# Kernel tuning notes

Measured on AMD Instinct MI355X. Metric: run time of the kernel, lower is better.

The kernel has to match this reference:

```python
import jax, jax.numpy as jnp
import numpy as np

B, S, T, H, D = 4, 128, 128, 256, 3


def setup_inputs() -> dict:
    key = jax.random.key(0)
    ks = jax.random.split(key, 10)
    s = 1.0 / np.sqrt(H).astype(np.float32)
    return {
        "src": jax.random.normal(ks[0], (B, S, H), jnp.float32),
        "trg": jax.random.normal(ks[1], (B, T, H), jnp.float32),
        "Wx_ih": jax.random.normal(ks[2], (D, H, H), jnp.float32) * s,
        "Wx_hh": jax.random.normal(ks[3], (D, H, H), jnp.float32) * s,
        "bx_ih": jax.random.normal(ks[4], (D, H), jnp.float32) * s,
        "bx_hh": jax.random.normal(ks[5], (D, H), jnp.float32) * s,
        "Wy_ih": jax.random.normal(ks[6], (D, H, H), jnp.float32) * s,
        "Wy_hh": jax.random.normal(ks[7], (D, H, H), jnp.float32) * s,
        "by_ih": jax.random.normal(ks[8], (D, H), jnp.float32) * s,
        "by_hh": jax.random.normal(ks[9], (D, H), jnp.float32) * s,
    }


def _grid_rnn(src, trg, Wx_ih, Wx_hh, bx_ih, bx_hh, Wy_ih, Wy_hh, by_ih, by_hh):
    dt = src.dtype
    hx = hy = None
    for d in range(D):
        if d == 0:
            xin = jnp.broadcast_to(src[:, :, None, :], (B, S, T, H))  # x_t(i,j)=src[i]
            yin = jnp.broadcast_to(trg[:, None, :, :], (B, S, T, H))  # y_t(i,j)=trg[j]
        else:
            xin, yin = hx, hy  # outputs of previous depth

        # ---- h_x: recurrence over rows i; state_x(i,j) = h_x(i-1, j-1),
        # with j==0 reading index -2 (Python wraparound) = h_x(i-1, T-1) -> jnp.roll.
        Wih, Whh, bih, bhh = Wx_ih[d], Wx_hh[d], bx_ih[d], bx_hh[d]

        def step_x(carry, x_i, Wih=Wih, Whh=Whh, bih=bih, bhh=bhh):
            state = jnp.roll(carry, 1, axis=1)  # [B,T,H]: state[j] = carry[j-1]
            h = jnp.tanh(x_i @ Wih.T + bih + state @ Whh.T + bhh)
            return h, h

        _, hx = jax.lax.scan(step_x, jnp.zeros((B, T, H), dt), jnp.swapaxes(xin, 0, 1))
        hx = jnp.swapaxes(hx, 0, 1)  # [B,S,T,H]

        # ---- h_y: recurrence over columns j; state_y(i,j) = h_y(i, j-1); rows independent.
        Wihy, Whhy, bihy, bhhy = Wy_ih[d], Wy_hh[d], by_ih[d], by_hh[d]

        def step_y(carry, y_j, Wih=Wihy, Whh=Whhy, bih=bihy, bhh=bhhy):
            h = jnp.tanh(y_j @ Wih.T + bih + carry @ Whh.T + bhh)
            return h, h

        _, hy = jax.lax.scan(step_y, jnp.zeros((B, S, H), dt), jnp.moveaxis(yin, 2, 0))
        hy = jnp.moveaxis(hy, 0, 2)  # [B,S,T,H]

    # final-depth output grid: slot 2j = h_x, slot 2j+1 = h_y
    return jnp.stack([hx, hy], axis=-2)  # [B,S,T,2,H]


def reference(src, trg, Wx_ih, Wx_hh, bx_ih, bx_hh, Wy_ih, Wy_hh, by_ih, by_hh):
    return _grid_rnn(src, trg, Wx_ih, Wx_hh, bx_ih, bx_hh, Wy_ih, Wy_hh, by_ih, by_hh)
```

## Files before the change

### kernel.cpp

```cpp
#include <hip/hip_runtime.h>


#define SS 128
#define TT 128
#define HH 256
#define GRID_ELEMS ((size_t)4 * 128 * 128 * 256)

typedef _Float16 half8 __attribute__((ext_vector_type(8)));
typedef float float4v __attribute__((ext_vector_type(4)));
typedef float float2v __attribute__((ext_vector_type(2)));

__device__ __forceinline__ float fast_tanh(float x) {
    float e = __expf(2.0f * x);
    return 1.0f - 2.0f / (e + 1.0f);
}

__device__ __forceinline__ unsigned short f2hbits(float x) {
    _Float16 h = (_Float16)x;
    return __builtin_bit_cast(unsigned short, h);
}

__device__ __forceinline__ float sel4(float4v v, int q) {
    float a = (q & 1) ? v[1] : v[0];
    float b = (q & 1) ? v[3] : v[2];
    return (q & 2) ? b : a;
}

__device__ __forceinline__ void lds_barrier() {
    asm volatile("s_waitcnt lgkmcnt(0)" ::: "memory");
    __builtin_amdgcn_s_barrier();
}

__device__ __forceinline__ half8 ldfrag_f32(const float* rowp, int k) {
    const float4v u0 = *(const float4v*)(rowp + k);
    const float4v u1 = *(const float4v*)(rowp + k + 4);
    half8 v;
#pragma unroll
    for (int e = 0; e < 4; ++e) { v[e] = (_Float16)u0[e]; v[4 + e] = (_Float16)u1[e]; }
    return v;
}

extern "C" __global__ void __launch_bounds__(512, 2)
grid_gemm0(const float* __restrict__ src, const float* __restrict__ trg,
           const float* __restrict__ Wx_ih, const float* __restrict__ Wy_ih,
           const float* __restrict__ bx_ih, const float* __restrict__ bx_hh,
           const float* __restrict__ by_ih, const float* __restrict__ by_hh,
           float* __restrict__ P0)
{
    __shared__ half8 aT[2048];

    const int tid  = threadIdx.x;
    const int lane = tid & 63;
    const int wv   = tid >> 6;
    const int quad = lane >> 4;
    const int l15  = lane & 15;

    const int bx    = blockIdx.x;
    const int dir   = bx >> 3;
    const int mtile = bx & 7;

    const float* Wih = dir ? Wy_ih : Wx_ih;
    const float* bih = dir ? by_ih : bx_ih;
    const float* bhh = dir ? by_hh : bx_hh;

    const int n_0 = (wv << 5) + l15;
    const int n_1 = n_0 + 16;

    half8 B0[8], B1[8];
    {
        const float* r0 = Wih + (size_t)n_0 * HH;
        const float* r1 = Wih + (size_t)n_1 * HH;
#pragma unroll
        for (int f = 0; f < 8; ++f) {
            const int k = (f << 5) + (quad << 3);
            B0[f] = ldfrag_f32(r0, k);
            B1[f] = ldfrag_f32(r1, k);
        }
    }
    const float bias0 = bih[n_0] + bhh[n_0];
    const float bias1 = bih[n_1] + bhh[n_1];

#pragma unroll
    for (int i = 0; i < 4; ++i) {
        const int c  = (tid << 2) + i;
        const int r  = c >> 5;
        const int kc = c & 31;
        const int R  = (mtile << 6) + r;
        const int b  = R >> 7, ii = R & 127;
        const float* row = (dir ? trg : src) + (size_t)((b << 7) + ii) * HH + (kc << 3);
        const float4v u0 = *(const float4v*)(row);
        const float4v u1 = *(const float4v*)(row + 4);
        half8 v;
#pragma unroll
        for (int e = 0; e < 4; ++e) { v[e] = (_Float16)u0[e]; v[4 + e] = (_Float16)u1[e]; }
        aT[((r >> 4) << 9) + ((kc >> 2) << 6) + ((kc & 3) << 4) + (r & 15)] = v;
    }
    __syncthreads();

#pragma unroll
    for (int msub = 0; msub < 4; ++msub) {
        half8 af[8];
#pragma unroll
        for (int f = 0; f < 8; ++f)
            af[f] = aT[(msub << 9) + (f << 6) + (quad << 4) + l15];

        float4v c0 = {bias0, bias0, bias0, bias0};
        float4v c1 = {bias1, bias1, bias1, bias1};
#pragma unroll
        for (int f = 0; f < 8; ++f) {
            c0 = __builtin_amdgcn_mfma_f32_16x16x32_f16(af[f], B0[f], c0, 0, 0, 0);
            c1 = __builtin_amdgcn_mfma_f32_16x16x32_f16(af[f], B1[f], c1, 0, 0, 0);
        }
#pragma unroll
        for (int r = 0; r < 4; ++r) {
            const int row = (msub << 4) + (quad << 2) + r;
            float* p = P0 + (size_t)dir * 131072 + (size_t)((mtile << 6) + row) * HH;
            p[n_0] = c0[r];
            p[n_1] = c1[r];
        }
    }
}

template <int DI>
__device__ __forceinline__ void rnn2f_body(
    const float* __restrict__ Wx_hh, const float* __restrict__ Wy_hh,
    const float* __restrict__ Wx_ih, const float* __restrict__ Wy_ih,
    const float* __restrict__ bx_ih, const float* __restrict__ bx_hh,
    const float* __restrict__ by_ih, const float* __restrict__ by_hh,
    float* __restrict__ out, const float* __restrict__ P0)
{
    __shared__ half8 aH[2][128];

    const int tid  = threadIdx.x;
    const int lane = tid & 63;
    const int wv   = tid >> 6;
    const int quad = lane >> 4;
    const int l15  = lane & 15;
    const int lrow = lane & 3;

    const int bid  = blockIdx.x;
    const int isY  = bid >= 128;
    const int g    = isY ? bid - 128 : bid;
    const int b    = g >> 5;
    const int c0   = (g & 31) << 2;
    const int slot = isY;

    const float* Whh  = (isY ? Wy_hh : Wx_hh) + (size_t)DI * HH * HH;
    const float* WihN = (isY ? Wy_ih : Wx_ih) + (size_t)(DI + 1) * HH * HH;
    const float* bihN = (isY ? by_ih : bx_ih) + (DI + 1) * HH;
    const float* bhhN = (isY ? by_hh : bx_hh) + (DI + 1) * HH;

    const int n_0 = (wv << 5) + l15;
    const int n_1 = n_0 + 16;

    half8 Bhh0[8], Bhh1[8], BN0[8], BN1[8];
    {
        const float* h0p = Whh  + (size_t)n_0 * HH;
        const float* h1p = Whh  + (size_t)n_1 * HH;
        const float* i0p = WihN + (size_t)n_0 * HH;
        const float* i1p = WihN + (size_t)n_1 * HH;
#pragma unroll
        for (int f = 0; f < 8; ++f) {
            const int k = (f << 5) + (quad << 3);
            Bhh0[f] = ldfrag_f32(h0p, k);
            Bhh1[f] = ldfrag_f32(h1p, k);
            BN0[f]  = ldfrag_f32(i0p, k);
            BN1[f]  = ldfrag_f32(i1p, k);
        }
    }
    const float biasN0 = bihN[n_0] + bhhN[n_0];
    const float biasN1 = bihN[n_1] + bhhN[n_1];

    int wj = isY ? 0 : ((c0 + quad) & 127);
    float* wp = out + (isY ? ((size_t)(b * SS + c0 + quad) * TT)
                           : ((size_t)b * SS * TT + wj)) * 2 * HH
                    + (size_t)slot * HH;

    float pA[4], pB[4];
    int rj = isY ? 0 : ((c0 + quad) & 127);
    const float* rp;
    if constexpr (DI == 0) {
        rp = P0 + (size_t)isY * 131072 + (size_t)b * 128 * HH;
    } else {
        rp = out + (isY ? ((size_t)(b * SS + c0 + quad) * TT)
                        : ((size_t)b * SS * TT + rj)) * 2 * HH
                 + (size_t)slot * HH;
    }
    auto rbump = [&]() {
        if constexpr (DI == 0) { rp += HH; }
        else if (isY)          { rp += 2 * HH; }
        else { rp += (size_t)(rj == 127 ? 1 : 129) * 2 * HH; rj = (rj + 1) & 127; }
    };
#pragma unroll
    for (int u = 0; u < 4; ++u) { pA[u] = rp[n_0]; pB[u] = rp[n_1]; rbump(); }

    if (tid < 128) {
        half8 z;
#pragma unroll
        for (int e = 0; e < 8; ++e) z[e] = (_Float16)0.f;
        aH[0][tid] = z;
    }
    __syncthreads();

    const int hi  = l15 >> 3;
    const int lo3 = l15 & 7;

    int buf = 0;
    for (int s4 = 0; s4 < 128; s4 += 4) {
#pragma unroll
        for (int u = 0; u < 4; ++u) {
            const int s = s4 + u;

            half8 ahr[8];
#pragma unroll
            for (int f = 0; f < 8; ++f)
                ahr[f] = aH[buf][(f << 4) + (quad << 2) + lrow];

            float4v ah0 = {0.f, 0.f, 0.f, 0.f};
            float4v ah1 = {0.f, 0.f, 0.f, 0.f};
            float4v pn0 = {biasN0, biasN0, biasN0, biasN0};
            float4v pn1 = {biasN1, biasN1, biasN1, biasN1};
            __builtin_amdgcn_s_setprio(1);
#pragma unroll
            for (int f = 0; f < 8; ++f) {
                ah0 = __builtin_amdgcn_mfma_f32_16x16x32_f16(ahr[f], Bhh0[f], ah0, 0, 0, 0);
                ah1 = __builtin_amdgcn_mfma_f32_16x16x32_f16(ahr[f], Bhh1[f], ah1, 0, 0, 0);
                pn0 = __builtin_amdgcn_mfma_f32_16x16x32_f16(ahr[f], BN0[f], pn0, 0, 0, 0);
                pn1 = __builtin_amdgcn_mfma_f32_16x16x32_f16(ahr[f], BN1[f], pn1, 0, 0, 0);
            }
            __builtin_amdgcn_s_setprio(0);

            if (s > 0) {
                wp[n_0] = sel4(pn0, quad);
                wp[n_1] = sel4(pn1, quad);
                if (isY) { wp += 2 * HH; }
                else { wp += (size_t)(wj == 127 ? 1 : 129) * 2 * HH; wj = (wj + 1) & 127; }
            }

            const float h0 = fast_tanh(sel4(ah0, quad) + pA[u]);
            const float h1 = fast_tanh(sel4(ah1, quad) + pB[u]);
            unsigned short* aHu = (unsigned short*)aH[buf ^ 1];
            aHu[(((wv << 4) + (hi << 2) + quad) << 3) + lo3]       = f2hbits(h0);
            aHu[(((wv << 4) + ((2 + hi) << 2) + quad) << 3) + lo3] = f2hbits(h1);

            if (s + 4 < 128) { pA[u] = rp[n_0]; pB[u] = rp[n_1]; rbump(); }

            lds_barrier();
            buf ^= 1;
        }
    }

    {
        half8 ahr[8];
#pragma unroll
        for (int f = 0; f < 8; ++f)
            ahr[f] = aH[buf][(f << 4) + (quad << 2) + lrow];
        float4v pn0 = {biasN0, biasN0, biasN0, biasN0};
        float4v pn1 = {biasN1, biasN1, biasN1, biasN1};
#pragma unroll
        for (int f = 0; f < 8; ++f) {
            pn0 = __builtin_amdgcn_mfma_f32_16x16x32_f16(ahr[f], BN0[f], pn0, 0, 0, 0);
            pn1 = __builtin_amdgcn_mfma_f32_16x16x32_f16(ahr[f], BN1[f], pn1, 0, 0, 0);
        }
        wp[n_0] = sel4(pn0, quad);
        wp[n_1] = sel4(pn1, quad);
    }
}

extern "C" __global__ void __launch_bounds__(512, 1)
grid_rnn2f_d0(const float* __restrict__ Wx_hh, const float* __restrict__ Wy_hh,
              const float* __restrict__ Wx_ih, const float* __restrict__ Wy_ih,
              const float* __restrict__ bx_ih, const float* __restrict__ bx_hh,
              const float* __restrict__ by_ih, const float* __restrict__ by_hh,
              float* __restrict__ out, const float* __restrict__ P0)
{ rnn2f_body<0>(Wx_hh, Wy_hh, Wx_ih, Wy_ih, bx_ih, bx_hh, by_ih, by_hh, out, P0); }

extern "C" __global__ void __launch_bounds__(512, 1)
grid_rnn2f_d1(const float* __restrict__ Wx_hh, const float* __restrict__ Wy_hh,
              const float* __restrict__ Wx_ih, const float* __restrict__ Wy_ih,
              const float* __restrict__ bx_ih, const float* __restrict__ bx_hh,
              const float* __restrict__ by_ih, const float* __restrict__ by_hh,
              float* __restrict__ out, const float* __restrict__ P0)
{ rnn2f_body<1>(Wx_hh, Wy_hh, Wx_ih, Wy_ih, bx_ih, bx_hh, by_ih, by_hh, out, P0); }

extern "C" __global__ void __launch_bounds__(512, 2)
grid_rnn2_last(const float* __restrict__ Wx_hh, const float* __restrict__ Wy_hh,
               float* __restrict__ out)
{
    __shared__ half8 aH[2][128];

    const int tid  = threadIdx.x;
    const int lane = tid & 63;
    const int wv   = tid >> 6;
    const int quad = lane >> 4;
    const int l15  = lane & 15;
    const int lrow = lane & 3;

    const int bid  = blockIdx.x;
    const int isY  = bid >= 128;
    const int g    = isY ? bid - 128 : bid;
    const int b    = g >> 5;
    const int c0   = (g & 31) << 2;
    const int slot = isY;

    const float* Whh = (isY ? Wy_hh : Wx_hh) + (size_t)2 * HH * HH;

    const int n_0 = (wv << 5) + l15;
    const int n_1 = n_0 + 16;

    half8 Bhh0[8], Bhh1[8];
    {
        const float* r0 = Whh + (size_t)n_0 * HH;
        const float* r1 = Whh + (size_t)n_1 * HH;
#pragma unroll
        for (int f = 0; f < 8; ++f) {
            const int k = (f << 5) + (quad << 3);
            Bhh0[f] = ldfrag_f32(r0, k);
            Bhh1[f] = ldfrag_f32(r1, k);
        }
    }

    float pA[4], pB[4];
    int rj = isY ? 0 : ((c0 + quad) & 127);
    const float* rp = out + (isY ? ((size_t)(b * SS + c0 + quad) * TT)
                                 : ((size_t)b * SS * TT + rj)) * 2 * HH
                          + (size_t)slot * HH;
    auto rbump = [&]() {
        if (isY) { rp += 2 * HH; }
        else { rp += (size_t)(rj == 127 ? 1 : 129) * 2 * HH; rj = (rj + 1) & 127; }
    };
#pragma unroll
    for (int u = 0; u < 4; ++u) { pA[u] = rp[n_0]; pB[u] = rp[n_1]; rbump(); }

    const int sm = tid >> 7;
    const int kk = (tid & 127) << 1;
    int sj = isY ? 0 : ((c0 + sm) & 127);
    float* sp = out + (isY ? ((size_t)(b * SS + c0 + sm) * TT)
                           : ((size_t)b * SS * TT + sj)) * 2 * HH
                    + (size_t)slot * HH + kk;
    const int rb32 = ((((kk >> 3) << 2) + sm) << 3 | (kk & 7)) >> 1;

    auto store_spread = [&](int bufi) {
        const unsigned int* a32 = (const unsigned int*)aH[bufi];
        const unsigned int w = a32[rb32];
        const _Float16 lo = __builtin_bit_cast(_Float16, (unsigned short)(w & 0xffff));
        const _Float16 hv = __builtin_bit_cast(_Float16, (unsigned short)(w >> 16));
        float2v t; t[0] = (float)lo; t[1] = (float)hv;
        *(float2v*)sp = t;
        if (isY) { sp += 2 * HH; }
        else { sp += (size_t)(sj == 127 ? 1 : 129) * 2 * HH; sj = (sj + 1) & 127; }
    };

    if (tid < 128) {
        half8 z;
#pragma unroll
        for (int e = 0; e < 8; ++e) z[e] = (_Float16)0.f;
        aH[0][tid] = z;
    }
    __syncthreads();

    const int hi  = l15 >> 3;
    const int lo3 = l15 & 7;

    int buf = 0;
    for (int s4 = 0; s4 < 128; s4 += 4) {
#pragma unroll
        for (int u = 0; u < 4; ++u) {
            const int s = s4 + u;

            if (s > 0) store_spread(buf);

            half8 ahr[8];
#pragma unroll
            for (int f = 0; f < 8; ++f)
                ahr[f] = aH[buf][(f << 4) + (quad << 2) + lrow];

            float4v ah0 = {0.f, 0.f, 0.f, 0.f};
            float4v ah1 = {0.f, 0.f, 0.f, 0.f};
            __builtin_amdgcn_s_setprio(1);
#pragma unroll
            for (int f = 0; f < 8; ++f) {
                ah0 = __builtin_amdgcn_mfma_f32_16x16x32_f16(ahr[f], Bhh0[f], ah0, 0, 0, 0);
                ah1 = __builtin_amdgcn_mfma_f32_16x16x32_f16(ahr[f], Bhh1[f], ah1, 0, 0, 0);
            }
            __builtin_amdgcn_s_setprio(0);

            const float h0 = fast_tanh(sel4(ah0, quad) + pA[u]);
            const float h1 = fast_tanh(sel4(ah1, quad) + pB[u]);
            unsigned short* aHu = (unsigned short*)aH[buf ^ 1];
            aHu[(((wv << 4) + (hi << 2) + quad) << 3) + lo3]       = f2hbits(h0);
            aHu[(((wv << 4) + ((2 + hi) << 2) + quad) << 3) + lo3] = f2hbits(h1);

            if (s + 4 < 128) { pA[u] = rp[n_0]; pB[u] = rp[n_1]; rbump(); }

            lds_barrier();
            buf ^= 1;
        }
    }

    store_spread(buf);
}

template <int DI>
__device__ __forceinline__ void grid_rnn_body_v1(
    const float* __restrict__ src, const float* __restrict__ trg,
    const float* __restrict__ Wx_ih, const float* __restrict__ Wx_hh,
    const float* __restrict__ bx_ih, const float* __restrict__ bx_hh,
    const float* __restrict__ Wy_ih, const float* __restrict__ Wy_hh,
    const float* __restrict__ by_ih, const float* __restrict__ by_hh,
    float* __restrict__ out)
{
    __shared__ half8 aX[2][128];
    __shared__ half8 aH[2][128];

    const int tid  = threadIdx.x;
    const int lane = tid & 63;
    const int wv   = tid >> 6;
    const int quad = lane >> 4;
    const int l15  = lane & 15;

    const int bid  = blockIdx.x;
    const int isY  = bid >= 128;
    const int g    = isY ? bid - 128 : bid;
    const int b    = g >> 5;
    const int c0   = (g & 31) << 2;
    const int slot = isY;

    const float* Wih = (isY ? Wy_ih : Wx_ih) + (size_t)DI * HH * HH;
    const float* Whh = (isY ? Wy_hh : Wx_hh) + (size_t)DI * HH * HH;
    const float* bih = (isY ? by_ih : bx_ih) + DI * HH;
    const float* bhh = (isY ? by_hh : bx_hh) + DI * HH;

    const int n_0 = (wv << 5) + l15;
    const int n_1 = n_0 + 16;

    half8 Bih0[8], Bih1[8], Bhh0[8], Bhh1[8];
    {
        const float* r0i = Wih + (size_t)n_0 * HH;
        const float* r1i = Wih + (size_t)n_1 * HH;
        const float* r0h = Whh + (size_t)n_0 * HH;
        const float* r1h = Whh + (size_t)n_1 * HH;
#pragma unroll
        for (int f = 0; f < 8; ++f) {
            const int k = (f << 5) + (quad << 3);
            Bih0[f] = ldfrag_f32(r0i, k);
            Bih1[f] = ldfrag_f32(r1i, k);
            Bhh0[f] = ldfrag_f32(r0h, k);
            Bhh1[f] = ldfrag_f32(r1h, k);
        }
    }
    const float bias0 = bih[n_0] + bhh[n_0];
    const float bias1 = bih[n_1] + bhh[n_1];

    const int sact = (tid < 128);
    const int cm   = tid & 3;
    const int ck0  = (tid >> 2) << 3;
    const int chc  = c0 + cm;

    auto stage_now = [&](int sn) -> half8 {
        const int i = isY ? chc : sn;
        const int j = isY ? sn : ((chc + sn) & 127);
        const size_t cell = (size_t)(b * SS + i) * TT + j;
        half8 v;
        if constexpr (DI == 0) {
            const float* row = isY ? (trg + (size_t)(b * TT + j) * HH)
                                   : (src + (size_t)(b * SS + i) * HH);
            const float4v u0 = *(const float4v*)(row + ck0);
            const float4v u1 = *(const float4v*)(row + ck0 + 4);
#pragma unroll
            for (int e = 0; e < 4; ++e) { v[e] = (_Float16)u0[e]; v[4 + e] = (_Float16)u1[e]; }
        } else {
            const float* row = out + cell * 2 * HH + (size_t)slot * HH + ck0;
            const float4v u0 = *(const float4v*)(row);
            const float4v u1 = *(const float4v*)(row + 4);
#pragma unroll
            for (int e = 0; e < 4; ++e) { v[e] = (_Float16)u0[e]; v[4 + e] = (_Float16)u1[e]; }
        }
        return v;
    };

    auto store_h = [&](int sp, int bufi) {
        const half8 v = aH[bufi][tid];
        const int i = isY ? chc : sp;
        const int j = isY ? sp : ((chc + sp) & 127);
        const size_t cell = (size_t)(b * SS + i) * TT + j;
        float* p = out + cell * 2 * HH + (size_t)slot * HH + ck0;
        float4v u0, u1;
#pragma unroll
        for (int e = 0; e < 4; ++e) { u0[e] = (float)v[e]; u1[e] = (float)v[4 + e]; }
        *(float4v*)p = u0;
        *(float4v*)(p + 4) = u1;
    };

    if (sact) {
        half8 z;
#pragma unroll
        for (int e = 0; e < 8; ++e) z[e] = (_Float16)0.f;
        aH[0][tid] = z;
        aX[0][tid] = stage_now(0);
    }
    __syncthreads();

    const int lrow = lane & 3;

    int buf = 0;
    for (int s = 0; s < 128; ++s) {
        if (s > 0 && sact) store_h(s - 1, buf);
        if (sact) {
            int t = s + 1; if (t > 127) t = 127;
            aX[buf ^ 1][tid] = stage_now(t);
        }

        half8 axr[8], ahr[8];
#pragma unroll
        for (int f = 0; f < 8; ++f) {
            const int e = (f << 4) + (quad << 2) + lrow;
            axr[f] = aX[buf][e];
            ahr[f] = aH[buf][e];
        }

        float4v ax0 = {bias0, bias0, bias0, bias0};
        float4v ax1 = {bias1, bias1, bias1, bias1};
        float4v ah0 = {0.f, 0.f, 0.f, 0.f};
        float4v ah1 = {0.f, 0.f, 0.f, 0.f};
#pragma unroll
        for (int f = 0; f < 8; ++f) {
            ax0 = __builtin_amdgcn_mfma_f32_16x16x32_f16(axr[f], Bih0[f], ax0, 0, 0, 0);
            ax1 = __builtin_amdgcn_mfma_f32_16x16x32_f16(axr[f], Bih1[f], ax1, 0, 0, 0);
            ah0 = __builtin_amdgcn_mfma_f32_16x16x32_f16(ahr[f], Bhh0[f], ah0, 0, 0, 0);
            ah1 = __builtin_amdgcn_mfma_f32_16x16x32_f16(ahr[f], Bhh1[f], ah1, 0, 0, 0);
        }

        if (quad == 0) {
            unsigned short* aHu = (unsigned short*)aH[buf ^ 1];
            const int lo3 = lane & 7;
            const int hi  = lane >> 3;
#pragma unroll
            for (int r = 0; r < 4; ++r) {
                const float h0 = fast_tanh(ax0[r] + ah0[r]);
                const float h1 = fast_tanh(ax1[r] + ah1[r]);
                aHu[(wv << 7) + (hi << 5) + (r << 3) + lo3]       = f2hbits(h0);
                aHu[(wv << 7) + ((2 + hi) << 5) + (r << 3) + lo3] = f2hbits(h1);
            }
        }

        lds_barrier();
        buf ^= 1;
    }

    if (sact) store_h(127, buf);
}

extern "C" __global__ void __launch_bounds__(512, 2)
grid_rnn_v1_d0(const float* __restrict__ src, const float* __restrict__ trg,
               const float* __restrict__ Wx_ih, const float* __restrict__ Wx_hh,
               const float* __restrict__ bx_ih, const float* __restrict__ bx_hh,
               const float* __restrict__ Wy_ih, const float* __restrict__ Wy_hh,
               const float* __restrict__ by_ih, const float* __restrict__ by_hh,
               float* __restrict__ out)
{ grid_rnn_body_v1<0>(src, trg, Wx_ih, Wx_hh, bx_ih, bx_hh, Wy_ih, Wy_hh, by_ih, by_hh, out); }

extern "C" __global__ void __launch_bounds__(512, 2)
grid_rnn_v1_d1(const float* __restrict__ src, const float* __restrict__ trg,
               const float* __restrict__ Wx_ih, const float* __restrict__ Wx_hh,
               const float* __restrict__ bx_ih, const float* __restrict__ bx_hh,
               const float* __restrict__ Wy_ih, const float* __restrict__ Wy_hh,
               const float* __restrict__ by_ih, const float* __restrict__ by_hh,
               float* __restrict__ out)
{ grid_rnn_body_v1<1>(src, trg, Wx_ih, Wx_hh, bx_ih, bx_hh, Wy_ih, Wy_hh, by_ih, by_hh, out); }

extern "C" __global__ void __launch_bounds__(512, 2)
grid_rnn_v1_d2(const float* __restrict__ src, const float* __restrict__ trg,
               const float* __restrict__ Wx_ih, const float* __restrict__ Wx_hh,
               const float* __restrict__ bx_ih, const float* __restrict__ bx_hh,
               const float* __restrict__ Wy_ih, const float* __restrict__ Wy_hh,
               const float* __restrict__ by_ih, const float* __restrict__ by_hh,
               float* __restrict__ out)
{ grid_rnn_body_v1<2>(src, trg, Wx_ih, Wx_hh, bx_ih, bx_hh, Wy_ih, Wy_hh, by_ih, by_hh, out); }

extern "C" void kernel_launch(void* const* d_in, const int* in_sizes, int n_in,
                              void* d_out, int out_size, void* d_ws, size_t ws_size,
                              hipStream_t stream) {
    const float* src   = (const float*)d_in[0];
    const float* trg   = (const float*)d_in[1];
    const float* Wx_ih = (const float*)d_in[2];
    const float* Wx_hh = (const float*)d_in[3];
    const float* bx_ih = (const float*)d_in[4];
    const float* bx_hh = (const float*)d_in[5];
    const float* Wy_ih = (const float*)d_in[6];
    const float* Wy_hh = (const float*)d_in[7];
    const float* by_ih = (const float*)d_in[8];
    const float* by_hh = (const float*)d_in[9];
    float* out = (float*)d_out;
    float* wsf = (float*)d_ws;

    const size_t needP0 = (size_t)2 * 131072 * sizeof(float);

    if (ws_size >= needP0) {
        hipLaunchKernelGGL(grid_gemm0, dim3(16), dim3(512), 0, stream,
                           src, trg, Wx_ih, Wy_ih, bx_ih, bx_hh, by_ih, by_hh, wsf);
        hipLaunchKernelGGL(grid_rnn2f_d0, dim3(256), dim3(512), 0, stream,
                           Wx_hh, Wy_hh, Wx_ih, Wy_ih, bx_ih, bx_hh, by_ih, by_hh,
                           out, (const float*)wsf);
        hipLaunchKernelGGL(grid_rnn2f_d1, dim3(256), dim3(512), 0, stream,
                           Wx_hh, Wy_hh, Wx_ih, Wy_ih, bx_ih, bx_hh, by_ih, by_hh,
                           out, (const float*)wsf);
        hipLaunchKernelGGL(grid_rnn2_last, dim3(256), dim3(512), 0, stream,
                           Wx_hh, Wy_hh, out);
    } else {
        hipLaunchKernelGGL(grid_rnn_v1_d0, dim3(256), dim3(512), 0, stream,
                           src, trg, Wx_ih, Wx_hh, bx_ih, bx_hh,
                           Wy_ih, Wy_hh, by_ih, by_hh, out);
        hipLaunchKernelGGL(grid_rnn_v1_d1, dim3(256), dim3(512), 0, stream,
                           src, trg, Wx_ih, Wx_hh, bx_ih, bx_hh,
                           Wy_ih, Wy_hh, by_ih, by_hh, out);
        hipLaunchKernelGGL(grid_rnn_v1_d2, dim3(256), dim3(512), 0, stream,
                           src, trg, Wx_ih, Wx_hh, bx_ih, bx_hh,
                           Wy_ih, Wy_hh, by_ih, by_hh, out);
    }
}
```

Baseline: 465.4 us.

## Defer next-depth input projection off the recurrence critical path via 8-deep LDS history

The fused recurrent kernel previously ran the next-depth input projection (BN MFMAs) inside every serial step, lengthening the dependent chain. It now keeps eight past hidden-state buffers in LDS and computes the projection for a group of four steps spread across the following four steps, two k-fragments per step, with deferred group stores. The recurrent MFMA chain is also split into two independent accumulators to shorten dependency latency, and the next P-value prefetch is hoisted earlier, with sched_barriers pinning the order. This costs more LDS and more complex index and store logic.

```diff
diff --git a/kernel.cpp b/kernel.cpp
--- a/kernel.cpp
+++ b/kernel.cpp
@@ -129,7 +129,7 @@
     const float* __restrict__ by_ih, const float* __restrict__ by_hh,
     float* __restrict__ out, const float* __restrict__ P0)
 {
-    __shared__ half8 aH[2][128];
+    __shared__ half8 aH[8][128];
 
     const int tid  = threadIdx.x;
     const int lane = tid & 63;
@@ -140,9 +140,9 @@
 
     const int bid  = blockIdx.x;
     const int isY  = bid >= 128;
-    const int g    = isY ? bid - 128 : bid;
-    const int b    = g >> 5;
-    const int c0   = (g & 31) << 2;
+    const int g0   = isY ? bid - 128 : bid;
+    const int b    = g0 >> 5;
+    const int c0   = (g0 & 31) << 2;
     const int slot = isY;
 
     const float* Whh  = (isY ? Wy_hh : Wx_hh) + (size_t)DI * HH * HH;
@@ -170,11 +170,6 @@
     }
     const float biasN0 = bihN[n_0] + bhhN[n_0];
     const float biasN1 = bihN[n_1] + bhhN[n_1];
-
-    int wj = isY ? 0 : ((c0 + quad) & 127);
-    float* wp = out + (isY ? ((size_t)(b * SS + c0 + quad) * TT)
-                           : ((size_t)b * SS * TT + wj)) * 2 * HH
-                    + (size_t)slot * HH;
 
     float pA[4], pB[4];
     int rj = isY ? 0 : ((c0 + quad) & 127);
@@ -194,6 +189,19 @@
 #pragma unroll
     for (int u = 0; u < 4; ++u) { pA[u] = rp[n_0]; pB[u] = rp[n_1]; rbump(); }
 
+    auto store_group = [&](int t4, const float4v& v0, const float4v& v1) {
+        const int t = t4 + quad;
+#pragma unroll
+        for (int r = 0; r < 4; ++r) {
+            const int ch = c0 + r;
+            const size_t cell = isY ? ((size_t)(b * SS + ch) * TT + t)
+                                    : ((size_t)(b * SS + t) * TT + ((ch + t) & 127));
+            float* p = out + cell * 2 * HH + (size_t)slot * HH;
+            p[n_0] = v0[r];
+            p[n_1] = v1[r];
+        }
+    };
+
     if (tid < 128) {
         half8 z;
 #pragma unroll
@@ -205,65 +213,78 @@
     const int hi  = l15 >> 3;
     const int lo3 = l15 & 7;
 
-    int buf = 0;
-    for (int s4 = 0; s4 < 128; s4 += 4) {
+    float4v pn0 = {0.f, 0.f, 0.f, 0.f}, pn1 = {0.f, 0.f, 0.f, 0.f};
+    float4v st0 = {0.f, 0.f, 0.f, 0.f}, st1 = {0.f, 0.f, 0.f, 0.f};
+
+    for (int g = 0; g < 32; ++g) {
 #pragma unroll
         for (int u = 0; u < 4; ++u) {
-            const int s = s4 + u;
-
+            const int s = (g << 2) + u;
+
+            if (u == 0 && g >= 2) store_group(((g - 2) << 2), st0, st1);
+
+            const float pAu = pA[u], pBu = pB[u];
+            if (s + 4 < 128) { pA[u] = rp[n_0]; pB[u] = rp[n_1]; rbump(); }
+
+            const half8* hb = aH[s & 7];
             half8 ahr[8];
 #pragma unroll
             for (int f = 0; f < 8; ++f)
-                ahr[f] = aH[buf][(f << 4) + (quad << 2) + lrow];
-
-            float4v ah0 = {0.f, 0.f, 0.f, 0.f};
-            float4v ah1 = {0.f, 0.f, 0.f, 0.f};
-            float4v pn0 = {biasN0, biasN0, biasN0, biasN0};
-            float4v pn1 = {biasN1, biasN1, biasN1, biasN1};
+                ahr[f] = hb[(f << 4) + (quad << 2) + lrow];
+
+            float4v a0a = {0.f,0.f,0.f,0.f}, a0b = {0.f,0.f,0.f,0.f};
+            float4v a1a = {0.f,0.f,0.f,0.f}, a1b = {0.f,0.f,0.f,0.f};
             __builtin_amdgcn_s_setprio(1);
 #pragma unroll
-            for (int f = 0; f < 8; ++f) {
-                ah0 = __builtin_amdgcn_mfma_f32_16x16x32_f16(ahr[f], Bhh0[f], ah0, 0, 0, 0);
-                ah1 = __builtin_amdgcn_mfma_f32_16x16x32_f16(ahr[f], Bhh1[f], ah1, 0, 0, 0);
-                pn0 = __builtin_amdgcn_mfma_f32_16x16x32_f16(ahr[f], BN0[f], pn0, 0, 0, 0);
-                pn1 = __builtin_amdgcn_mfma_f32_16x16x32_f16(ahr[f], BN1[f], pn1, 0, 0, 0);
+            for (int f = 0; f < 4; ++f) {
+                a0a = __builtin_amdgcn_mfma_f32_16x16x32_f16(ahr[f],     Bhh0[f],     a0a, 0, 0, 0);
+                a1a = __builtin_amdgcn_mfma_f32_16x16x32_f16(ahr[f],     Bhh1[f],     a1a, 0, 0, 0);
+                a0b = __builtin_amdgcn_mfma_f32_16x16x32_f16(ahr[f + 4], Bhh0[f + 4], a0b, 0, 0, 0);
+                a1b = __builtin_amdgcn_mfma_f32_16x16x32_f16(ahr[f + 4], Bhh1[f + 4], a1b, 0, 0, 0);
             }
             __builtin_amdgcn_s_setprio(0);
 
-            if (s > 0) {
-                wp[n_0] = sel4(pn0, quad);
-                wp[n_1] = sel4(pn1, quad);
-                if (isY) { wp += 2 * HH; }
-                else { wp += (size_t)(wj == 127 ? 1 : 129) * 2 * HH; wj = (wj + 1) & 127; }
-            }
-
-            const float h0 = fast_tanh(sel4(ah0, quad) + pA[u]);
-            const float h1 = fast_tanh(sel4(ah1, quad) + pB[u]);
-            unsigned short* aHu = (unsigned short*)aH[buf ^ 1];
+            const float h0 = fast_tanh(sel4(a0a, quad) + sel4(a0b, quad) + pAu);
+            const float h1 = fast_tanh(sel4(a1a, quad) + sel4(a1b, quad) + pBu);
+            unsigned short* aHu = (unsigned short*)aH[(s + 1) & 7];
             aHu[(((wv << 4) + (hi << 2) + quad) << 3) + lo3]       = f2hbits(h0);
             aHu[(((wv << 4) + ((2 + hi) << 2) + quad) << 3) + lo3] = f2hbits(h1);
 
-            if (s + 4 < 128) { pA[u] = rp[n_0]; pB[u] = rp[n_1]; rbump(); }
+            __builtin_amdgcn_sched_barrier(0);
+
+            if (g >= 1) {
+                if (u == 0) {
+                    pn0 = float4v{biasN0, biasN0, biasN0, biasN0};
+                    pn1 = float4v{biasN1, biasN1, biasN1, biasN1};
+                }
+                const half8* ib = aH[((g << 2) - 3 + (l15 >> 2)) & 7];
+#pragma unroll
+                for (int ff = 0; ff < 2; ++ff) {
+                    const int f = (u << 1) + ff;
+                    const half8 af = ib[(f << 4) + (quad << 2) + (l15 & 3)];
+                    pn0 = __builtin_amdgcn_mfma_f32_16x16x32_f16(af, BN0[f], pn0, 0, 0, 0);
+                    pn1 = __builtin_amdgcn_mfma_f32_16x16x32_f16(af, BN1[f], pn1, 0, 0, 0);
+                }
+                if (u == 3) { st0 = pn0; st1 = pn1; }
+            }
 
             lds_barrier();
-            buf ^= 1;
-        }
-    }
-
+            __builtin_amdgcn_sched_barrier(0);
+        }
+    }
+
+    store_group((30 << 2), st0, st1);
     {
-        half8 ahr[8];
-#pragma unroll
-        for (int f = 0; f < 8; ++f)
-            ahr[f] = aH[buf][(f << 4) + (quad << 2) + lrow];
-        float4v pn0 = {biasN0, biasN0, biasN0, biasN0};
-        float4v pn1 = {biasN1, biasN1, biasN1, biasN1};
-#pragma unroll
-        for (int f = 0; f < 8; ++f) {
-            pn0 = __builtin_amdgcn_mfma_f32_16x16x32_f16(ahr[f], BN0[f], pn0, 0, 0, 0);
-            pn1 = __builtin_amdgcn_mfma_f32_16x16x32_f16(ahr[f], BN1[f], pn1, 0, 0, 0);
-        }
-        wp[n_0] = sel4(pn0, quad);
-        wp[n_1] = sel4(pn1, quad);
+        float4v p0 = {biasN0, biasN0, biasN0, biasN0};
+        float4v p1 = {biasN1, biasN1, biasN1, biasN1};
+        const half8* ib = aH[(5 + (l15 >> 2)) & 7];
+#pragma unroll
+        for (int f = 0; f < 8; ++f) {
+            const half8 af = ib[(f << 4) + (quad << 2) + (l15 & 3)];
+            p0 = __builtin_amdgcn_mfma_f32_16x16x32_f16(af, BN0[f], p0, 0, 0, 0);
+            p1 = __builtin_amdgcn_mfma_f32_16x16x32_f16(af, BN1[f], p1, 0, 0, 0);
+        }
+        store_group((31 << 2), p0, p1);
     }
 }
 
@@ -370,30 +391,34 @@
 
             if (s > 0) store_spread(buf);
 
+            const float pAu = pA[u], pBu = pB[u];
+            if (s + 4 < 128) { pA[u] = rp[n_0]; pB[u] = rp[n_1]; rbump(); }
+
             half8 ahr[8];
 #pragma unroll
             for (int f = 0; f < 8; ++f)
                 ahr[f] = aH[buf][(f << 4) + (quad << 2) + lrow];
 
-            float4v ah0 = {0.f, 0.f, 0.f, 0.f};
-            float4v ah1 = {0.f, 0.f, 0.f, 0.f};
+            float4v a0a = {0.f,0.f,0.f,0.f}, a0b = {0.f,0.f,0.f,0.f};
+            float4v a1a = {0.f,0.f,0.f,0.f}, a1b = {0.f,0.f,0.f,0.f};
             __builtin_amdgcn_s_setprio(1);
 #pragma unroll
-            for (int f = 0; f < 8; ++f) {
-                ah0 = __builtin_amdgcn_mfma_f32_16x16x32_f16(ahr[f], Bhh0[f], ah0, 0, 0, 0);
-                ah1 = __builtin_amdgcn_mfma_f32_16x16x32_f16(ahr[f], Bhh1[f], ah1, 0, 0, 0);
+            for (int f = 0; f < 4; ++f) {
+                a0a = __builtin_amdgcn_mfma_f32_16x16x32_f16(ahr[f],     Bhh0[f],     a0a, 0, 0, 0);
+                a1a = __builtin_amdgcn_mfma_f32_16x16x32_f16(ahr[f],     Bhh1[f],     a1a, 0, 0, 0);
+                a0b = __builtin_amdgcn_mfma_f32_16x16x32_f16(ahr[f + 4], Bhh0[f + 4], a0b, 0, 0, 0);
+                a1b = __builtin_amdgcn_mfma_f32_16x16x32_f16(ahr[f + 4], Bhh1[f + 4], a1b, 0, 0, 0);
             }
             __builtin_amdgcn_s_setprio(0);
 
-            const float h0 = fast_tanh(sel4(ah0, quad) + pA[u]);
-            const float h1 = fast_tanh(sel4(ah1, quad) + pB[u]);
+            const float h0 = fast_tanh(sel4(a0a, quad) + sel4(a0b, quad) + pAu);
+            const float h1 = fast_tanh(sel4(a1a, quad) + sel4(a1b, quad) + pBu);
             unsigned short* aHu = (unsigned short*)aH[buf ^ 1];
             aHu[(((wv << 4) + (hi << 2) + quad) << 3) + lo3]       = f2hbits(h0);
             aHu[(((wv << 4) + ((2 + hi) << 2) + quad) << 3) + lo3] = f2hbits(h1);
 
-            if (s + 4 < 128) { pA[u] = rp[n_0]; pB[u] = rp[n_1]; rbump(); }
-
             lds_barrier();
+            __builtin_amdgcn_sched_barrier(0);
             buf ^= 1;
         }
     }
```

Result: faster. 418.4 us, median of 2 (-10.1%).
